# Performance work log

Measured on AMD Instinct MI355X. Metric: run time of the kernel, lower is better.

Reference implementation:

```python
import jax, jax.numpy as jnp
import numpy as np

B, N, D = 4, 4096, 1024
H, DH = 16, 64
EPS = 1e-5


def setup_inputs() -> dict:
    key = jax.random.key(0)
    ks = jax.random.split(key, 4)
    x = jax.random.normal(ks[0], (B, N, D), dtype=jnp.float32)
    w_qkv = jax.random.normal(ks[1], (D, 3 * H * DH), dtype=jnp.float32) * 0.02
    # per-head LayerNorm affine params (one LayerNorm(dim_head) per head)
    gamma_k = jnp.ones((H, DH), dtype=jnp.float32)
    beta_k = jnp.zeros((H, DH), dtype=jnp.float32)
    gamma_v = jnp.ones((H, DH), dtype=jnp.float32)
    beta_v = jnp.zeros((H, DH), dtype=jnp.float32)
    w_out = jax.random.normal(ks[2], (H * DH, D), dtype=jnp.float32) * 0.02
    b_out = jnp.zeros((D,), dtype=jnp.float32)
    return {"x": x, "w_qkv": w_qkv, "gamma_k": gamma_k, "beta_k": beta_k,
            "gamma_v": gamma_v, "beta_v": beta_v, "w_out": w_out, "b_out": b_out}


def _per_head_layernorm(t, gamma, beta):
    # t: [b, h, n, d]; gamma/beta: [h, d] (distinct affine per head)
    mu = jnp.mean(t, axis=-1, keepdims=True)
    var = jnp.mean(jnp.square(t - mu), axis=-1, keepdims=True)  # biased, as torch LayerNorm
    tn = (t - mu) * jax.lax.rsqrt(var + EPS)
    return tn * gamma[None, :, None, :] + beta[None, :, None, :]


def reference(x, w_qkv, gamma_k, beta_k, gamma_v, beta_v, w_out, b_out):
    b, n, _ = x.shape
    h, dh = gamma_k.shape
    qkv = jnp.einsum('bnd,de->bne', x, w_qkv)  # [b, n, 3*h*dh]
    q, k, v = jnp.split(qkv, 3, axis=-1)

    def to_heads(t):  # b n (h d) -> b h n d
        return t.reshape(b, n, h, dh).transpose(0, 2, 1, 3)

    q, k, v = to_heads(q), to_heads(k), to_heads(v)
    k = _per_head_layernorm(k, gamma_k, beta_k)
    v = _per_head_layernorm(v, gamma_v, beta_v)
    # linear attention: scores = k^T v / n  -> [b, h, d, d]
    scores = jnp.einsum('bhnd,bhne->bhde', k, v) / n
    out = jnp.einsum('bhnd,bhde->bhne', q, scores)  # [b, h, n, d]
    out = out.transpose(0, 2, 1, 3).reshape(b, n, h * dh)
    return jnp.einsum('bne,ed->bnd', out, w_out) + b_out
```

## Files before the change

### kernel.cpp

```cpp
#include <hip/hip_runtime.h>

typedef __attribute__((ext_vector_type(4))) float f32x4;
typedef __attribute__((ext_vector_type(8))) short s16x8;

#define DEV static __device__ __forceinline__

typedef __attribute__((address_space(3))) void lds_t;
typedef __attribute__((address_space(1))) void gbl_t;

DEV void gload_lds16(const void* g, void* l) {
    __builtin_amdgcn_global_load_lds((gbl_t*)g, (lds_t*)l, 16, 0, 0);
}

DEV ushort f2bf(float f) {
    unsigned u = __float_as_uint(f);
    u += 0x7fffu + ((u >> 16) & 1u);
    return (ushort)(u >> 16);
}
DEV float bf2f(ushort h) { return __uint_as_float(((unsigned)h) << 16); }

#define FULLBAR() do {                              \
    __builtin_amdgcn_sched_barrier(0);              \
    asm volatile("" ::: "memory");                  \
    __builtin_amdgcn_s_barrier();                   \
    asm volatile("" ::: "memory");                  \
    __builtin_amdgcn_sched_barrier(0);              \
} while (0)

#define WAITVM(n) asm volatile("s_waitcnt vmcnt(" #n ")" ::: "memory")
#define LGKM0() asm volatile("s_waitcnt lgkmcnt(0)" ::: "memory")

__global__ void pack_x_k(const float* __restrict__ x, ushort* __restrict__ xb, int n4) {
    int stride = gridDim.x * blockDim.x;
    for (int i = blockIdx.x * blockDim.x + threadIdx.x; i < n4; i += stride) {
        float4 v = reinterpret_cast<const float4*>(x)[i];
        ushort4 o;
        o.x = f2bf(v.x); o.y = f2bf(v.y); o.z = f2bf(v.z); o.w = f2bf(v.w);
        reinterpret_cast<ushort4*>(xb)[i] = o;
    }
}

__global__ void prep_w_k(const float* __restrict__ wqkv, const float* __restrict__ wout,
                         ushort* __restrict__ wqb, ushort* __restrict__ wkvT,
                         ushort* __restrict__ woutT) {
    __shared__ float tile[32][33];
    const int bx = blockIdx.x, by = blockIdx.y;
    const int tx = threadIdx.x, ty = threadIdx.y;
    if (bx < 64) {
        int bxo = bx * 32, byr = by * 32;
        int blk = bxo >> 8, grp = (bxo >> 6) & 3, d0 = bxo & 63;
        int h = blk * 2 + (grp >> 1);
        int src = 1024 + (grp & 1) * 1024 + h * 64 + d0;
#pragma unroll
        for (int i = 0; i < 32; i += 8)
            tile[ty + i][tx] = wqkv[(size_t)(byr + ty + i) * 3072 + src + tx];
        __syncthreads();
#pragma unroll
        for (int i = 0; i < 32; i += 8)
            wkvT[(size_t)(bxo + ty + i) * 1024 + byr + tx] = f2bf(tile[tx][ty + i]);
    } else if (bx < 96) {
        int bxo = (bx - 64) * 32, byr = by * 32;
#pragma unroll
        for (int i = 0; i < 32; i += 8)
            tile[ty + i][tx] = wout[(size_t)(byr + ty + i) * 1024 + bxo + tx];
        __syncthreads();
#pragma unroll
        for (int i = 0; i < 32; i += 8)
            woutT[(size_t)(bxo + ty + i) * 1024 + byr + tx] = f2bf(tile[tx][ty + i]);
    } else {
        int t = ty * 32 + tx;
        int i = ((bx - 96) * 32 + by) * 256 + t;
        int r = i >> 8, c4 = i & 255;
        float4 v = *reinterpret_cast<const float4*>(wqkv + (size_t)r * 3072 + c4 * 4);
        ushort4 u;
        u.x = f2bf(v.x); u.y = f2bf(v.y); u.z = f2bf(v.z); u.w = f2bf(v.w);
        *reinterpret_cast<ushort4*>(wqb + (size_t)r * 1024 + c4 * 4) = u;
    }
}

template <int MODE>
__global__ __launch_bounds__(512, 1) void gemm_bt_k(
    const ushort* __restrict__ A, const ushort* __restrict__ Bt,
    int Nn, size_t b_stride,
    float* __restrict__ scp,
    const float* __restrict__ gk, const float* __restrict__ bk,
    const float* __restrict__ gv, const float* __restrict__ bv,
    const float* __restrict__ bias, float* __restrict__ outf)
{
    __shared__ __align__(16) ushort SH[65536];
    const int t = threadIdx.x;
    const int w = t >> 6, lane = t & 63;
    const int wr = w >> 2, wc = w & 3;
    const int lrow = lane & 15, kh = lane >> 4;

    int bid = blockIdx.y * gridDim.x + blockIdx.x;
    int C8 = (gridDim.x * gridDim.y) >> 3;
    int nid = (bid & 7) * C8 + (bid >> 3);
    int n0 = (nid % gridDim.x) * 256;
    int m0 = (nid / gridDim.x) * 256;

    const ushort* Bte = (MODE == 1) ? Bt + (size_t)(m0 >> 12) * b_stride : Bt;

    const int srow8 = w * 8 + (lane >> 3);
    const int scol = ((lane & 7) ^ ((lane >> 3) & 7)) * 8;

    const int g0 = ((kh) ^ (lrow & 7)) * 8;
    const int g1 = ((4 + kh) ^ (lrow & 7)) * 8;

    f32x4 acc[8][4] = {};
    s16x8 bfr[4][2];
    s16x8 af[8];

    auto STAGE_A = [&](int kt, int s, int h) {
        ushort* As = SH + s * 32768;
        const ushort* Ag = A + (size_t)(m0 + h * 128 + srow8) * 1024 + kt * 64 + scol;
        gload_lds16(Ag,                     As + (h * 128 + w * 8) * 64);
        gload_lds16(Ag + (size_t)64 * 1024, As + (h * 128 + 64 + w * 8) * 64);
    };
    auto STAGE_B = [&](int kt, int s, int h) {
        ushort* Bs = SH + s * 32768 + 16384;
        const ushort* Bg = Bte + (size_t)(n0 + h * 128 + srow8) * 1024 + kt * 64 + scol;
        gload_lds16(Bg,                     Bs + (h * 128 + w * 8) * 64);
        gload_lds16(Bg + (size_t)64 * 1024, Bs + (h * 128 + 64 + w * 8) * 64);
    };

    STAGE_A(0, 0, 0); STAGE_A(0, 0, 1);
    STAGE_B(0, 0, 0); STAGE_B(0, 0, 1);
    STAGE_B(1, 1, 0); STAGE_B(1, 1, 1);

    for (int kt = 0; kt < 16; ++kt) {
        const int p = kt & 1, q = p ^ 1;
        const ushort* As = SH + p * 32768;
        const ushort* Bs = As + 16384;

        if (kt < 15) { WAITVM(4); } else { WAITVM(0); }
        FULLBAR();

#pragma unroll
        for (int ni = 0; ni < 4; ni++) {
            const int r = (wc * 64 + ni * 16 + lrow) * 64;
            bfr[ni][0] = *reinterpret_cast<const s16x8*>(&Bs[r + g0]);
            bfr[ni][1] = *reinterpret_cast<const s16x8*>(&Bs[r + g1]);
        }
#pragma unroll
        for (int mi = 0; mi < 8; mi++)
            af[mi] = *reinterpret_cast<const s16x8*>(&As[(wr * 128 + mi * 16 + lrow) * 64 + g0]);
        if (kt + 1 < 16) { STAGE_A(kt + 1, q, 0); STAGE_A(kt + 1, q, 1); }

        __builtin_amdgcn_s_setprio(1);
#pragma unroll
        for (int mi = 0; mi < 8; mi++)
#pragma unroll
            for (int ni = 0; ni < 4; ni++)
                acc[mi][ni] = __builtin_amdgcn_mfma_f32_16x16x32_bf16(af[mi], bfr[ni][0], acc[mi][ni], 0, 0, 0);
        __builtin_amdgcn_s_setprio(0);

        LGKM0();
        FULLBAR();

        if (kt + 2 < 16) { STAGE_B(kt + 2, p, 0); STAGE_B(kt + 2, p, 1); }
#pragma unroll
        for (int mi = 0; mi < 8; mi++)
            af[mi] = *reinterpret_cast<const s16x8*>(&As[(wr * 128 + mi * 16 + lrow) * 64 + g1]);

        __builtin_amdgcn_s_setprio(1);
#pragma unroll
        for (int mi = 0; mi < 8; mi++)
#pragma unroll
            for (int ni = 0; ni < 4; ni++)
                acc[mi][ni] = __builtin_amdgcn_mfma_f32_16x16x32_bf16(af[mi], bfr[ni][1], acc[mi][ni], 0, 0, 0);
        __builtin_amdgcn_s_setprio(0);
    }

    if (MODE == 0) {
        const int i_nb = n0 >> 8;
        const int h = i_nb * 2 + (wc >> 1);
        const int is_k = ((wc & 1) == 0);
        const float* g  = is_k ? gk : gv;
        const float* bb = is_k ? bk : bv;
        float gr[4], br[4];
#pragma unroll
        for (int ni = 0; ni < 4; ni++) {
            gr[ni] = g[h * 64 + ni * 16 + lrow];
            br[ni] = bb[h * 64 + ni * 16 + lrow];
        }
        __syncthreads();
        ushort* kvl = SH + wc * 16384;
#pragma unroll
        for (int mi = 0; mi < 8; mi++) {
            float muA[4], invA[4];
#pragma unroll
            for (int j = 0; j < 4; j++) {
                float s = acc[mi][0][j] + acc[mi][1][j] + acc[mi][2][j] + acc[mi][3][j];
                s += __shfl_xor(s, 1, 64);
                s += __shfl_xor(s, 2, 64);
                s += __shfl_xor(s, 4, 64);
                s += __shfl_xor(s, 8, 64);
                float mu = s * (1.f / 64.f);
                float t2 = 0.f;
#pragma unroll
                for (int ni = 0; ni < 4; ni++) {
                    float dd = acc[mi][ni][j] - mu;
                    t2 += dd * dd;
                }
                t2 += __shfl_xor(t2, 1, 64);
                t2 += __shfl_xor(t2, 2, 64);
                t2 += __shfl_xor(t2, 4, 64);
                t2 += __shfl_xor(t2, 8, 64);
                muA[j] = mu;
                invA[j] = rsqrtf(t2 * (1.f / 64.f) + 1e-5f);
            }
            const int nbase = wr * 128 + mi * 16 + kh * 4;
            const int gnb = nbase >> 3;
#pragma unroll
            for (int ni = 0; ni < 4; ni++) {
                ushort4 o;
                o.x = f2bf((acc[mi][ni][0] - muA[0]) * invA[0] * gr[ni] + br[ni]);
                o.y = f2bf((acc[mi][ni][1] - muA[1]) * invA[1] * gr[ni] + br[ni]);
                o.z = f2bf((acc[mi][ni][2] - muA[2]) * invA[2] * gr[ni] + br[ni]);
                o.w = f2bf((acc[mi][ni][3] - muA[3]) * invA[3] * gr[ni] + br[ni]);
                const int c = ni * 16 + lrow;
                const int gn = gnb ^ (c & 31);
                *reinterpret_cast<ushort4*>(&kvl[c * 256 + gn * 8 + (kh & 1) * 4]) = o;
            }
        }
        __syncthreads();
        const int hp = w >> 2, T = w & 3;
        const ushort* Ak = SH + (hp * 2) * 16384;
        const ushort* Bv = SH + (hp * 2 + 1) * 16384;
        const int arow = T * 16 + lrow;
        f32x4 sacc[4] = {};
#pragma unroll
        for (int ks = 0; ks < 8; ++ks) {
            const int gnr = ks * 4 + kh;
            s16x8 afk = *reinterpret_cast<const s16x8*>(
                &Ak[arow * 256 + ((gnr ^ (arow & 31)) * 8)]);
#pragma unroll
            for (int ni = 0; ni < 4; ni++) {
                const int erow = ni * 16 + lrow;
                s16x8 bfv = *reinterpret_cast<const s16x8*>(
                    &Bv[erow * 256 + ((gnr ^ (erow & 31)) * 8)]);
                sacc[ni] = __builtin_amdgcn_mfma_f32_16x16x32_bf16(afk, bfv, sacc[ni], 0, 0, 0);
            }
        }
        const int bh = (m0 >> 12) * 16 + i_nb * 2 + hp;
        float* scb = scp + (size_t)bh * 4096;
        const float scale = 1.f / 4096.f;
#pragma unroll
        for (int ni = 0; ni < 4; ni++)
#pragma unroll
            for (int j = 0; j < 4; j++) {
                const int d = T * 16 + kh * 4 + j;
                const int e = ni * 16 + lrow;
                atomicAdd(&scb[d * 64 + e], sacc[ni][j] * scale);
            }
    } else {
#pragma unroll
        for (int mi = 0; mi < 8; mi++)
#pragma unroll
            for (int ni = 0; ni < 4; ni++) {
                int e = n0 + wc * 64 + ni * 16 + lrow;
                float bv2 = bias[e];
#pragma unroll
                for (int j = 0; j < 4; j++) {
                    int m = m0 + wr * 128 + mi * 16 + kh * 4 + j;
                    outf[(size_t)m * Nn + e] = acc[mi][ni][j] + bv2;
                }
            }
    }
}

__global__ __launch_bounds__(256) void fold_k(const ushort* __restrict__ A,
                                              const ushort* __restrict__ Bt,
                                              ushort* __restrict__ out)
{
    __shared__ __align__(16) ushort SH2[24576];
    const int t = threadIdx.x;
    const int w = t >> 6, lane = t & 63;
    const int wm = w >> 1, wn = w & 1;
    const int lrow = lane & 15, kh = lane >> 4;
    const int n0 = blockIdx.x * 128, m0 = blockIdx.y * 128;

    const int srow0 = w * 32 + (lane >> 2);
    const int scolSwz = (((lane & 3) ^ ((lane >> 3) & 3)) * 8);

    f32x4 acc[4][4] = {};

    auto STAGE = [&](int kt, int s) {
        ushort* As = SH2 + s * 8192;
        ushort* Bs = As + 4096;
        const ushort* Ag = A  + (size_t)(m0 + srow0) * 1024 + kt * 32 + scolSwz;
        const ushort* Bg = Bt + (size_t)(n0 + srow0) * 1024 + kt * 32 + scolSwz;
        gload_lds16(Ag,             As + w * 1024);
        gload_lds16(Bg,             Bs + w * 1024);
        gload_lds16(Ag + 16 * 1024, As + w * 1024 + 512);
        gload_lds16(Bg + 16 * 1024, Bs + w * 1024 + 512);
    };

    const int rdoff = (kh ^ ((lrow >> 1) & 3)) * 8;

    auto COMPUTE = [&](int s) {
        const ushort* As = SH2 + s * 8192;
        const ushort* Bs = As + 4096;
        s16x8 af[4], bfr[4];
#pragma unroll
        for (int mi = 0; mi < 4; mi++)
            af[mi] = *reinterpret_cast<const s16x8*>(&As[(wm * 64 + mi * 16 + lrow) * 32 + rdoff]);
#pragma unroll
        for (int ni = 0; ni < 4; ni++)
            bfr[ni] = *reinterpret_cast<const s16x8*>(&Bs[(wn * 64 + ni * 16 + lrow) * 32 + rdoff]);
#pragma unroll
        for (int mi = 0; mi < 4; mi++)
#pragma unroll
            for (int ni = 0; ni < 4; ni++)
                acc[mi][ni] = __builtin_amdgcn_mfma_f32_16x16x32_bf16(af[mi], bfr[ni], acc[mi][ni], 0, 0, 0);
    };

    STAGE(0, 0);
    STAGE(1, 1);
    int ss = 2, sc_ = 0;
    for (int kt = 0; kt < 30; ++kt) {
        STAGE(kt + 2, ss);
        ss = (ss == 2) ? 0 : ss + 1;
        WAITVM(8);
        FULLBAR();
        COMPUTE(sc_);
        sc_ = (sc_ == 2) ? 0 : sc_ + 1;
        FULLBAR();
    }
    WAITVM(4); FULLBAR(); COMPUTE(0); FULLBAR();
    WAITVM(0); FULLBAR(); COMPUTE(1);

#pragma unroll
    for (int mi = 0; mi < 4; mi++)
#pragma unroll
        for (int ni = 0; ni < 4; ni++) {
            int e = n0 + wn * 64 + ni * 16 + lrow;
#pragma unroll
            for (int j = 0; j < 4; j++) {
                int m = m0 + wm * 64 + mi * 16 + kh * 4 + j;
                out[(size_t)m * 1024 + e] = f2bf(acc[mi][ni][j]);
            }
        }
}

__global__ __launch_bounds__(256) void wprime_k(const float* __restrict__ sc,
                                                const ushort* __restrict__ woutT,
                                                ushort* __restrict__ wpT)
{
    __shared__ float scl[64][65];
    __shared__ ushort wl[128][72];
    int bh = blockIdx.y;
    int b = bh >> 4, h = bh & 15;
    int f0 = blockIdx.x * 128;
    int t = threadIdx.x;
    for (int i = t; i < 4096; i += 256) {
        int d2 = i >> 6, e = i & 63;
        scl[e][d2] = sc[(size_t)bh * 4096 + i];
    }
    for (int i = t; i < 1024; i += 256) {
        int fl = i >> 3, c = i & 7;
        *reinterpret_cast<int4*>(&wl[fl][c * 8]) =
            *reinterpret_cast<const int4*>(woutT + (size_t)(f0 + fl) * 1024 + h * 64 + c * 8);
    }
    __syncthreads();
    int dd = (t & 7) * 8;
    int fl0 = t >> 3;
#pragma unroll
    for (int fi = 0; fi < 4; ++fi) {
        int fl = fi * 32 + fl0;
        float acc[8] = {};
        for (int e = 0; e < 64; ++e) {
            float wv = bf2f(wl[fl][e]);
#pragma unroll
            for (int i = 0; i < 8; ++i)
                acc[i] = fmaf(wv, scl[e][dd + i], acc[i]);
        }
        ushort4 o0, o1;
        o0.x = f2bf(acc[0]); o0.y = f2bf(acc[1]); o0.z = f2bf(acc[2]); o0.w = f2bf(acc[3]);
        o1.x = f2bf(acc[4]); o1.y = f2bf(acc[5]); o1.z = f2bf(acc[6]); o1.w = f2bf(acc[7]);
        ushort* op = wpT + ((size_t)b * 1024 + f0 + fl) * 1024 + h * 64 + dd;
        *reinterpret_cast<ushort4*>(op) = o0;
        *reinterpret_cast<ushort4*>(op + 4) = o1;
    }
}

extern "C" void kernel_launch(void* const* d_in, const int* in_sizes, int n_in,
                              void* d_out, int out_size, void* d_ws, size_t ws_size,
                              hipStream_t stream)
{
    const float* x       = (const float*)d_in[0];
    const float* w_qkv   = (const float*)d_in[1];
    const float* gamma_k = (const float*)d_in[2];
    const float* beta_k  = (const float*)d_in[3];
    const float* gamma_v = (const float*)d_in[4];
    const float* beta_v  = (const float*)d_in[5];
    const float* w_out   = (const float*)d_in[6];
    const float* b_out   = (const float*)d_in[7];
    float* out = (float*)d_out;

    char* ws = (char*)d_ws;
    const size_t MB = 1024 * 1024;
    ushort* xb    = (ushort*)(ws);
    ushort* wkvT  = (ushort*)(ws + 32 * MB);
    ushort* woutT = (ushort*)(ws + 38 * MB);
    ushort* wqb   = (ushort*)(ws + 40 * MB);
    float*  sc    = (float*)(ws + 48 * MB);
    ushort* wpT   = (ushort*)(ws + 56 * MB);
    ushort* fT    = (ushort*)(ws + 64 * MB);

    hipMemsetAsync(sc, 0, 64 * 4096 * sizeof(float), stream);
    pack_x_k<<<2048, 256, 0, stream>>>(x, xb, 16384 * 1024 / 4);
    prep_w_k<<<dim3(128, 32), dim3(32, 8), 0, stream>>>(w_qkv, w_out, wqb, wkvT, woutT);
    gemm_bt_k<0><<<dim3(8, 64), 512, 0, stream>>>(xb, wkvT, 2048, 0,
                                                  sc,
                                                  gamma_k, beta_k, gamma_v, beta_v,
                                                  nullptr, nullptr);
    wprime_k<<<dim3(8, 64), 256, 0, stream>>>(sc, woutT, wpT);
    fold_k<<<dim3(8, 32), 256, 0, stream>>>(wpT, wqb, fT);
    gemm_bt_k<1><<<dim3(4, 64), 512, 0, stream>>>(xb, fT, 1024, (size_t)1048576,
                                                  nullptr,
                                                  nullptr, nullptr, nullptr, nullptr,
                                                  b_out, out);
}
```

Measured before the change: 193.9 us.

## Fuse wprime and fold kernels per head; merge x packing into weight prep

Replaces the separate wprime_k (scalar FMA computing W_out·scores into a bf16 intermediate) and fold_k (a pipelined GEMM of that intermediate with W_q) with one wfold_k kernel. Per head it computes the small product with MFMA into LDS and immediately accumulates against W_q, so the wpT intermediate never goes through global memory. It also folds the x-to-bf16 packing into the weight prep kernel, saving a launch. The trade-off is that the fused kernel reads W_q and W_out straight from global memory without async LDS staging or pipelining, and it synchronises three times per head across 16 sequential head iterations.

```diff
diff --git a/kernel.cpp b/kernel.cpp
--- a/kernel.cpp
+++ b/kernel.cpp
@@ -30,19 +30,10 @@
 #define WAITVM(n) asm volatile("s_waitcnt vmcnt(" #n ")" ::: "memory")
 #define LGKM0() asm volatile("s_waitcnt lgkmcnt(0)" ::: "memory")
 
-__global__ void pack_x_k(const float* __restrict__ x, ushort* __restrict__ xb, int n4) {
-    int stride = gridDim.x * blockDim.x;
-    for (int i = blockIdx.x * blockDim.x + threadIdx.x; i < n4; i += stride) {
-        float4 v = reinterpret_cast<const float4*>(x)[i];
-        ushort4 o;
-        o.x = f2bf(v.x); o.y = f2bf(v.y); o.z = f2bf(v.z); o.w = f2bf(v.w);
-        reinterpret_cast<ushort4*>(xb)[i] = o;
-    }
-}
-
-__global__ void prep_w_k(const float* __restrict__ wqkv, const float* __restrict__ wout,
-                         ushort* __restrict__ wqb, ushort* __restrict__ wkvT,
-                         ushort* __restrict__ woutT) {
+__global__ void prep_k(const float* __restrict__ x, const float* __restrict__ wqkv,
+                       const float* __restrict__ wout,
+                       ushort* __restrict__ xb, ushort* __restrict__ wqb,
+                       ushort* __restrict__ wkvT, ushort* __restrict__ woutT) {
     __shared__ float tile[32][33];
     const int bx = blockIdx.x, by = blockIdx.y;
     const int tx = threadIdx.x, ty = threadIdx.y;
@@ -67,7 +58,7 @@
 #pragma unroll
         for (int i = 0; i < 32; i += 8)
             woutT[(size_t)(bxo + ty + i) * 1024 + byr + tx] = f2bf(tile[tx][ty + i]);
-    } else {
+    } else if (bx < 128) {
         int t = ty * 32 + tx;
         int i = ((bx - 96) * 32 + by) * 256 + t;
         int r = i >> 8, c4 = i & 255;
@@ -75,6 +66,13 @@
         ushort4 u;
         u.x = f2bf(v.x); u.y = f2bf(v.y); u.z = f2bf(v.z); u.w = f2bf(v.w);
         *reinterpret_cast<ushort4*>(wqb + (size_t)r * 1024 + c4 * 4) = u;
+    } else {
+        int t = ty * 32 + tx;
+        int i = ((bx - 128) * 32 + by) * 256 + t;
+        float4 v = reinterpret_cast<const float4*>(x)[i];
+        ushort4 u;
+        u.x = f2bf(v.x); u.y = f2bf(v.y); u.z = f2bf(v.z); u.w = f2bf(v.w);
+        reinterpret_cast<ushort4*>(xb)[i] = u;
     }
 }
 
@@ -270,119 +268,72 @@
     }
 }
 
-__global__ __launch_bounds__(256) void fold_k(const ushort* __restrict__ A,
-                                              const ushort* __restrict__ Bt,
-                                              ushort* __restrict__ out)
+__global__ __launch_bounds__(512) void wfold_k(const float* __restrict__ sc,
+                                               const ushort* __restrict__ woutT,
+                                               const ushort* __restrict__ wqb,
+                                               ushort* __restrict__ fT)
 {
-    __shared__ __align__(16) ushort SH2[24576];
+    __shared__ ushort Sl[64 * 72];
+    __shared__ ushort Tl[128 * 72];
     const int t = threadIdx.x;
     const int w = t >> 6, lane = t & 63;
-    const int wm = w >> 1, wn = w & 1;
     const int lrow = lane & 15, kh = lane >> 4;
-    const int n0 = blockIdx.x * 128, m0 = blockIdx.y * 128;
-
-    const int srow0 = w * 32 + (lane >> 2);
-    const int scolSwz = (((lane & 3) ^ ((lane >> 3) & 3)) * 8);
-
-    f32x4 acc[4][4] = {};
-
-    auto STAGE = [&](int kt, int s) {
-        ushort* As = SH2 + s * 8192;
-        ushort* Bs = As + 4096;
-        const ushort* Ag = A  + (size_t)(m0 + srow0) * 1024 + kt * 32 + scolSwz;
-        const ushort* Bg = Bt + (size_t)(n0 + srow0) * 1024 + kt * 32 + scolSwz;
-        gload_lds16(Ag,             As + w * 1024);
-        gload_lds16(Bg,             Bs + w * 1024);
-        gload_lds16(Ag + 16 * 1024, As + w * 1024 + 512);
-        gload_lds16(Bg + 16 * 1024, Bs + w * 1024 + 512);
-    };
-
-    const int rdoff = (kh ^ ((lrow >> 1) & 3)) * 8;
-
-    auto COMPUTE = [&](int s) {
-        const ushort* As = SH2 + s * 8192;
-        const ushort* Bs = As + 4096;
-        s16x8 af[4], bfr[4];
-#pragma unroll
-        for (int mi = 0; mi < 4; mi++)
-            af[mi] = *reinterpret_cast<const s16x8*>(&As[(wm * 64 + mi * 16 + lrow) * 32 + rdoff]);
-#pragma unroll
-        for (int ni = 0; ni < 4; ni++)
-            bfr[ni] = *reinterpret_cast<const s16x8*>(&Bs[(wn * 64 + ni * 16 + lrow) * 32 + rdoff]);
-#pragma unroll
-        for (int mi = 0; mi < 4; mi++)
+    const int c0 = blockIdx.x * 128;
+    const int m0 = blockIdx.y * 128;
+    const int b = m0 >> 10;
+
+    f32x4 facc[8] = {};
+    const int Frow = m0 + w * 16 + lrow;
+
+    for (int h = 0; h < 16; ++h) {
+        const float* sb = sc + ((size_t)(b * 16 + h)) * 4096;
+#pragma unroll
+        for (int ii = 0; ii < 8; ++ii) {
+            int idx = t * 8 + ii;
+            Sl[(idx >> 6) * 72 + (idx & 63)] = f2bf(sb[idx]);
+        }
+        __syncthreads();
+        {
+            f32x4 tacc[4] = {};
+            s16x8 a0 = *reinterpret_cast<const s16x8*>(
+                woutT + (size_t)(Frow & 1023) * 1024 + h * 64 + kh * 8);
+            s16x8 a1 = *reinterpret_cast<const s16x8*>(
+                woutT + (size_t)(Frow & 1023) * 1024 + h * 64 + 32 + kh * 8);
+#pragma unroll
+            for (int ni = 0; ni < 4; ni++) {
+                const ushort* srow = &Sl[(ni * 16 + lrow) * 72];
+                s16x8 b0 = *reinterpret_cast<const s16x8*>(srow + kh * 8);
+                s16x8 b1 = *reinterpret_cast<const s16x8*>(srow + 32 + kh * 8);
+                tacc[ni] = __builtin_amdgcn_mfma_f32_16x16x32_bf16(a0, b0, tacc[ni], 0, 0, 0);
+                tacc[ni] = __builtin_amdgcn_mfma_f32_16x16x32_bf16(a1, b1, tacc[ni], 0, 0, 0);
+            }
 #pragma unroll
             for (int ni = 0; ni < 4; ni++)
-                acc[mi][ni] = __builtin_amdgcn_mfma_f32_16x16x32_bf16(af[mi], bfr[ni], acc[mi][ni], 0, 0, 0);
-    };
-
-    STAGE(0, 0);
-    STAGE(1, 1);
-    int ss = 2, sc_ = 0;
-    for (int kt = 0; kt < 30; ++kt) {
-        STAGE(kt + 2, ss);
-        ss = (ss == 2) ? 0 : ss + 1;
-        WAITVM(8);
-        FULLBAR();
-        COMPUTE(sc_);
-        sc_ = (sc_ == 2) ? 0 : sc_ + 1;
-        FULLBAR();
+#pragma unroll
+                for (int j = 0; j < 4; j++)
+                    Tl[(w * 16 + kh * 4 + j) * 72 + ni * 16 + lrow] = f2bf(tacc[ni][j]);
+        }
+        __syncthreads();
+        {
+            s16x8 a0 = *reinterpret_cast<const s16x8*>(&Tl[(w * 16 + lrow) * 72 + kh * 8]);
+            s16x8 a1 = *reinterpret_cast<const s16x8*>(&Tl[(w * 16 + lrow) * 72 + 32 + kh * 8]);
+#pragma unroll
+            for (int ni = 0; ni < 8; ni++) {
+                const ushort* qrow = wqb + (size_t)(c0 + ni * 16 + lrow) * 1024 + h * 64;
+                s16x8 b0 = *reinterpret_cast<const s16x8*>(qrow + kh * 8);
+                s16x8 b1 = *reinterpret_cast<const s16x8*>(qrow + 32 + kh * 8);
+                facc[ni] = __builtin_amdgcn_mfma_f32_16x16x32_bf16(a0, b0, facc[ni], 0, 0, 0);
+                facc[ni] = __builtin_amdgcn_mfma_f32_16x16x32_bf16(a1, b1, facc[ni], 0, 0, 0);
+            }
+        }
+        __syncthreads();
     }
-    WAITVM(4); FULLBAR(); COMPUTE(0); FULLBAR();
-    WAITVM(0); FULLBAR(); COMPUTE(1);
-
-#pragma unroll
-    for (int mi = 0; mi < 4; mi++)
-#pragma unroll
-        for (int ni = 0; ni < 4; ni++) {
-            int e = n0 + wn * 64 + ni * 16 + lrow;
-#pragma unroll
-            for (int j = 0; j < 4; j++) {
-                int m = m0 + wm * 64 + mi * 16 + kh * 4 + j;
-                out[(size_t)m * 1024 + e] = f2bf(acc[mi][ni][j]);
-            }
-        }
-}
-
-__global__ __launch_bounds__(256) void wprime_k(const float* __restrict__ sc,
-                                                const ushort* __restrict__ woutT,
-                                                ushort* __restrict__ wpT)
-{
-    __shared__ float scl[64][65];
-    __shared__ ushort wl[128][72];
-    int bh = blockIdx.y;
-    int b = bh >> 4, h = bh & 15;
-    int f0 = blockIdx.x * 128;
-    int t = threadIdx.x;
-    for (int i = t; i < 4096; i += 256) {
-        int d2 = i >> 6, e = i & 63;
-        scl[e][d2] = sc[(size_t)bh * 4096 + i];
-    }
-    for (int i = t; i < 1024; i += 256) {
-        int fl = i >> 3, c = i & 7;
-        *reinterpret_cast<int4*>(&wl[fl][c * 8]) =
-            *reinterpret_cast<const int4*>(woutT + (size_t)(f0 + fl) * 1024 + h * 64 + c * 8);
-    }
-    __syncthreads();
-    int dd = (t & 7) * 8;
-    int fl0 = t >> 3;
-#pragma unroll
-    for (int fi = 0; fi < 4; ++fi) {
-        int fl = fi * 32 + fl0;
-        float acc[8] = {};
-        for (int e = 0; e < 64; ++e) {
-            float wv = bf2f(wl[fl][e]);
-#pragma unroll
-            for (int i = 0; i < 8; ++i)
-                acc[i] = fmaf(wv, scl[e][dd + i], acc[i]);
-        }
-        ushort4 o0, o1;
-        o0.x = f2bf(acc[0]); o0.y = f2bf(acc[1]); o0.z = f2bf(acc[2]); o0.w = f2bf(acc[3]);
-        o1.x = f2bf(acc[4]); o1.y = f2bf(acc[5]); o1.z = f2bf(acc[6]); o1.w = f2bf(acc[7]);
-        ushort* op = wpT + ((size_t)b * 1024 + f0 + fl) * 1024 + h * 64 + dd;
-        *reinterpret_cast<ushort4*>(op) = o0;
-        *reinterpret_cast<ushort4*>(op + 4) = o1;
-    }
+#pragma unroll
+    for (int ni = 0; ni < 8; ni++)
+#pragma unroll
+        for (int j = 0; j < 4; j++)
+            fT[(size_t)(m0 + w * 16 + kh * 4 + j) * 1024 + c0 + ni * 16 + lrow] =
+                f2bf(facc[ni][j]);
 }
 
 extern "C" void kernel_launch(void* const* d_in, const int* in_sizes, int n_in,
@@ -406,18 +357,15 @@
     ushort* woutT = (ushort*)(ws + 38 * MB);
     ushort* wqb   = (ushort*)(ws + 40 * MB);
     float*  sc    = (float*)(ws + 48 * MB);
-    ushort* wpT   = (ushort*)(ws + 56 * MB);
     ushort* fT    = (ushort*)(ws + 64 * MB);
 
     hipMemsetAsync(sc, 0, 64 * 4096 * sizeof(float), stream);
-    pack_x_k<<<2048, 256, 0, stream>>>(x, xb, 16384 * 1024 / 4);
-    prep_w_k<<<dim3(128, 32), dim3(32, 8), 0, stream>>>(w_qkv, w_out, wqb, wkvT, woutT);
+    prep_k<<<dim3(640, 32), dim3(32, 8), 0, stream>>>(x, w_qkv, w_out, xb, wqb, wkvT, woutT);
     gemm_bt_k<0><<<dim3(8, 64), 512, 0, stream>>>(xb, wkvT, 2048, 0,
                                                   sc,
                                                   gamma_k, beta_k, gamma_v, beta_v,
                                                   nullptr, nullptr);
-    wprime_k<<<dim3(8, 64), 256, 0, stream>>>(sc, woutT, wpT);
-    fold_k<<<dim3(8, 32), 256, 0, stream>>>(wpT, wqb, fT);
+    wfold_k<<<dim3(8, 32), 512, 0, stream>>>(sc, woutT, wqb, fT);
     gemm_bt_k<1><<<dim3(4, 64), 512, 0, stream>>>(xb, fT, 1024, (size_t)1048576,
                                                   nullptr,
                                                   nullptr, nullptr, nullptr, nullptr,
```

After: 239.2 us. 23.4% more time.
